# Kernel tuning notes

Measured on AMD Instinct MI355X. Metric: run time of the kernel, lower is better.

Reference implementation:

```python
import jax, jax.numpy as jnp
import numpy as np

DIM = 256
HEADS = 8
HEAD_DIM = DIM // HEADS
WS = 8
EPS = 1e-5


def layernorm(x, g, b):
    mu = jnp.mean(x, axis=-1, keepdims=True)
    var = jnp.var(x, axis=-1, keepdims=True)
    return (x - mu) * jax.lax.rsqrt(var + EPS) * g + b


def partition_windows(x, ws):
    B, H, W, C = x.shape
    x = x.reshape(B, H // ws, ws, W // ws, ws, C)
    x = jnp.transpose(x, (0, 1, 3, 2, 4, 5))
    return x.reshape(B * (H // ws) * (W // ws), ws * ws, C)


def unpartition_windows(x, ws, B, H, W):
    C = x.shape[-1]
    x = x.reshape(B, H // ws, W // ws, ws, ws, C)
    x = jnp.transpose(x, (0, 1, 3, 2, 4, 5))
    return x.reshape(B, H, W, C)


def setup_inputs() -> dict:
    key = jax.random.key(0)
    ks = jax.random.split(key, 14)
    B, H, W, C = 16, 64, 64, DIM
    s_in = 1.0 / np.sqrt(C)
    s_hid = 1.0 / np.sqrt(4 * C)
    return {
        "x": jax.random.normal(ks[0], (B, H, W, C), jnp.float32),
        "ln1_g": jnp.ones((C,), jnp.float32),
        "ln1_b": jnp.zeros((C,), jnp.float32),
        "qkv_w": jax.random.uniform(ks[1], (3 * C, C), jnp.float32, -s_in, s_in),
        "qkv_b": jax.random.uniform(ks[2], (3 * C,), jnp.float32, -s_in, s_in),
        "proj_w": jax.random.uniform(ks[3], (C, C), jnp.float32, -s_in, s_in),
        "proj_b": jax.random.uniform(ks[4], (C,), jnp.float32, -s_in, s_in),
        "ln2_g": jnp.ones((C,), jnp.float32),
        "ln2_b": jnp.zeros((C,), jnp.float32),
        "ffn_w1": jax.random.uniform(ks[5], (4 * C, C), jnp.float32, -s_in, s_in),
        "ffn_b1": jax.random.uniform(ks[6], (4 * C,), jnp.float32, -s_in, s_in),
        "ffn_w2": jax.random.uniform(ks[7], (C, 4 * C), jnp.float32, -s_hid, s_hid),
        "ffn_b2": jax.random.uniform(ks[8], (C,), jnp.float32, -s_hid, s_hid),
    }


def attention(blocks, qkv_w, qkv_b, proj_w, proj_b):
    # blocks: [Bn, N, C]
    Bn, N, C = blocks.shape
    qkv = blocks @ qkv_w.T + qkv_b  # [Bn, N, 3C]
    qkv = qkv.reshape(Bn, N, 3, HEADS, HEAD_DIM)
    q, k, v = qkv[:, :, 0], qkv[:, :, 1], qkv[:, :, 2]  # each [Bn, N, h, d]
    # Faithful to the source: q @ k^T over the last two dims -> head-x-head scores per token
    scores = jnp.einsum("bnhd,bngd->bnhg", q, k) / np.sqrt(HEAD_DIM)
    attn = jax.nn.softmax(scores, axis=-1)
    out = jnp.einsum("bnhg,bngd->bnhd", attn, v).reshape(Bn, N, C)
    return out @ proj_w.T + proj_b


def reference(x, ln1_g, ln1_b, qkv_w, qkv_b, proj_w, proj_b,
              ln2_g, ln2_b, ffn_w1, ffn_b1, ffn_w2, ffn_b2):
    B, H, W, C = x.shape
    x_ = layernorm(x, ln1_g, ln1_b)
    blocks = partition_windows(x_, WS)  # [B*nW, ws*ws, C]
    out = attention(blocks, qkv_w, qkv_b, proj_w, proj_b)
    x = x + unpartition_windows(out, WS, B, H, W)
    x_ = layernorm(x, ln2_g, ln2_b)
    x_ = jax.nn.relu(x_ @ ffn_w1.T + ffn_b1) @ ffn_w2.T + ffn_b2
    return x + x_
```

## Files before the change

kernel.cpp:

```cpp
#include <hip/hip_runtime.h>
#include <hip/hip_bf16.h>
#include <stdint.h>

typedef float f32x4 __attribute__((ext_vector_type(4)));
typedef __bf16 bf16x8 __attribute__((ext_vector_type(8)));
typedef unsigned short ushort8 __attribute__((ext_vector_type(8)));

__device__ __forceinline__ float bf2f(unsigned short u) {
    unsigned int x = ((unsigned int)u) << 16;
    return __builtin_bit_cast(float, x);
}
__device__ __forceinline__ unsigned short f2bf(float f) {
    unsigned int x = __builtin_bit_cast(unsigned int, f);
    unsigned int lsb = (x >> 16) & 1u;
    x += 0x7fffu + lsb;
    return (unsigned short)(x >> 16);
}

#define GLL16(gptr, lptr)                                                      \
    __builtin_amdgcn_global_load_lds(                                          \
        (const __attribute__((address_space(1))) void*)(gptr),                 \
        (__attribute__((address_space(3))) void*)(lptr), 16, 0, 0)

__global__ __launch_bounds__(256) void cvt4_kernel(
    const float* __restrict__ w0, const float* __restrict__ w1,
    const float* __restrict__ w2, const float* __restrict__ w3,
    unsigned short* __restrict__ dst)
{
    const int i = blockIdx.x * 256 + threadIdx.x;
    const float* s; int off;
    if      (i <  49152) { s = w0; off = 0; }
    else if (i <  65536) { s = w1; off = 49152; }
    else if (i < 131072) { s = w2; off = 65536; }
    else                 { s = w3; off = 131072; }
    f32x4 v = ((const f32x4*)s)[i - off];
    ushort4 o;
    o.x = f2bf(v.x); o.y = f2bf(v.y); o.z = f2bf(v.z); o.w = f2bf(v.w);
    ((ushort4*)dst)[i] = o;
}

__global__ __launch_bounds__(256) void ln_kernel(
    const float* __restrict__ x, const float* __restrict__ g,
    const float* __restrict__ b, unsigned short* __restrict__ y)
{
    const int lane = threadIdx.x & 63, wave = threadIdx.x >> 6;
    const size_t tok = (size_t)blockIdx.x * 4 + wave;
    f32x4 v = *(const f32x4*)(x + tok * 256 + lane * 4);
    float s = v.x + v.y + v.z + v.w;
    float q = v.x * v.x + v.y * v.y + v.z * v.z + v.w * v.w;
#pragma unroll
    for (int o = 32; o; o >>= 1) {
        s += __shfl_xor(s, o, 64);
        q += __shfl_xor(q, o, 64);
    }
    float mean = s * (1.f / 256.f);
    float var  = q * (1.f / 256.f) - mean * mean;
    float rstd = rsqrtf(var + 1e-5f);
    f32x4 gr = *(const f32x4*)(g + lane * 4);
    f32x4 br = *(const f32x4*)(b + lane * 4);
    ushort4 o4;
    o4.x = f2bf((v.x - mean) * rstd * gr.x + br.x);
    o4.y = f2bf((v.y - mean) * rstd * gr.y + br.y);
    o4.z = f2bf((v.z - mean) * rstd * gr.z + br.z);
    o4.w = f2bf((v.w - mean) * rstd * gr.w + br.w);
    *(ushort4*)(y + tok * 256 + lane * 4) = o4;
}

template <int RELU, int HASRES, int OUTF32>
__global__ __launch_bounds__(256) void gemm_bt(
    const unsigned short* __restrict__ A,
    const unsigned short* __restrict__ W,
    const float* __restrict__ bias,
    const float* res,
    void* Cv,
    int M, int N, int K, int nby)
{
    __shared__ __align__(16) unsigned short As[128 * 64];
    __shared__ __align__(16) unsigned short Bs[128 * 64];

    const int t    = threadIdx.x;
    const int id   = blockIdx.x;
    const int xcd  = id & 7;
    const int sl   = id >> 3;
    const int by   = sl % nby;
    const int bx   = (sl / nby) * 8 + xcd;
    const int m0   = bx * 128;
    const int n0   = by * 128;
    const int lane = t & 63;
    const int wave = t >> 6;
    const int wm = wave & 1, wn = wave >> 1;
    const int lr = lane & 15, kc = lane >> 4;

    f32x4 acc[4][4] = {};

    const int rA   = t >> 3;
    const int gcol = ((t & 7) ^ (rA & 7)) * 8;
    const unsigned short* gA = A + (size_t)(m0 + rA) * K + gcol;
    const unsigned short* gB = W + (size_t)(n0 + rA) * K + gcol;

    for (int k0 = 0; k0 < K; k0 += 64) {
#pragma unroll
        for (int w = 0; w < 4; ++w) {
            GLL16(gA + (size_t)(w * 32) * K + k0, &As[(w * 256 + t) * 8]);
            GLL16(gB + (size_t)(w * 32) * K + k0, &Bs[(w * 256 + t) * 8]);
        }
        __syncthreads();

#pragma unroll
        for (int hh = 0; hh < 2; ++hh) {
            bf16x8 af[4], bf[4];
#pragma unroll
            for (int i = 0; i < 4; ++i) {
                const int ra = wm * 64 + i * 16 + lr;
                const int rb = wn * 64 + i * 16 + lr;
                af[i] = *(const bf16x8*)&As[ra * 64 + ((hh * 4 + kc) ^ (ra & 7)) * 8];
                bf[i] = *(const bf16x8*)&Bs[rb * 64 + ((hh * 4 + kc) ^ (rb & 7)) * 8];
            }
#pragma unroll
            for (int i = 0; i < 4; ++i)
#pragma unroll
                for (int j = 0; j < 4; ++j)
                    acc[i][j] = __builtin_amdgcn_mfma_f32_16x16x32_bf16(
                        af[i], bf[j], acc[i][j], 0, 0, 0);
        }
        __syncthreads();
    }

    float* Cf = (float*)Cv;
    unsigned short* Cb = (unsigned short*)Cv;
    const int row0 = m0 + wm * 64;
    const int col0 = n0 + wn * 64;
    const int cl = lane & 15;
    const int rq = (lane >> 4) * 4;
#pragma unroll
    for (int i = 0; i < 4; ++i) {
#pragma unroll
        for (int j = 0; j < 4; ++j) {
            const int col = col0 + j * 16 + cl;
            const float bv = bias[col];
#pragma unroll
            for (int r = 0; r < 4; ++r) {
                const int row = row0 + i * 16 + rq + r;
                float v = acc[i][j][r] + bv;
                if (RELU) v = fmaxf(v, 0.f);
                const size_t o = (size_t)row * N + col;
                if (HASRES) v += res[o];
                if (OUTF32) Cf[o] = v;
                else        Cb[o] = f2bf(v);
            }
        }
    }
}

__global__ __launch_bounds__(256) void attn_headmix(
    const unsigned short* __restrict__ qkv,
    unsigned short* __restrict__ out,
    int T)
{
    const int lane = threadIdx.x & 63, wave = threadIdx.x >> 6;
    const int tok = blockIdx.x * 4 + wave;
    if (tok >= T) return;
    const unsigned short* base = qkv + (size_t)tok * 768;
    const int h = lane >> 3, g = lane & 7;

    float s = 0.f;
#pragma unroll
    for (int d8 = 0; d8 < 4; ++d8) {
        ushort4 qa = *(const ushort4*)(base + h * 32 + d8 * 8);
        ushort4 qb = *(const ushort4*)(base + h * 32 + d8 * 8 + 4);
        ushort4 ka = *(const ushort4*)(base + 256 + g * 32 + d8 * 8);
        ushort4 kb = *(const ushort4*)(base + 256 + g * 32 + d8 * 8 + 4);
        s += bf2f(qa.x) * bf2f(ka.x) + bf2f(qa.y) * bf2f(ka.y)
           + bf2f(qa.z) * bf2f(ka.z) + bf2f(qa.w) * bf2f(ka.w)
           + bf2f(qb.x) * bf2f(kb.x) + bf2f(qb.y) * bf2f(kb.y)
           + bf2f(qb.z) * bf2f(kb.z) + bf2f(qb.w) * bf2f(kb.w);
    }
    s *= 0.17677669529663687f;

    float mx = s;
#pragma unroll
    for (int o = 1; o < 8; o <<= 1) mx = fmaxf(mx, __shfl_xor(mx, o, 64));
    float e = __expf(s - mx);
    float sum = e;
#pragma unroll
    for (int o = 1; o < 8; o <<= 1) sum += __shfl_xor(sum, o, 64);
    const float a = e / sum;

    float o0 = 0.f, o1 = 0.f, o2 = 0.f, o3 = 0.f;
#pragma unroll
    for (int gg = 0; gg < 8; ++gg) {
        const float ag = __shfl(a, (lane & 56) | gg, 64);
        ushort4 vv = *(const ushort4*)(base + 512 + gg * 32 + g * 4);
        o0 += ag * bf2f(vv.x);
        o1 += ag * bf2f(vv.y);
        o2 += ag * bf2f(vv.z);
        o3 += ag * bf2f(vv.w);
    }
    ushort4 ov;
    ov.x = f2bf(o0); ov.y = f2bf(o1); ov.z = f2bf(o2); ov.w = f2bf(o3);
    *(ushort4*)(out + (size_t)tok * 256 + lane * 4) = ov;
}

__global__ __launch_bounds__(512, 2) void ffn_fused(
    float* xo,
    const float* __restrict__ ln2_g, const float* __restrict__ ln2_b,
    const unsigned short* __restrict__ w1,
    const float* __restrict__ b1p,
    const unsigned short* __restrict__ w2,
    const float* __restrict__ b2p)
{
    __shared__ __align__(16) unsigned short U[32768];
    __shared__ __align__(16) unsigned short W1a[16384];
    __shared__ __align__(16) unsigned short W2a[16384];
    __shared__ __align__(16) unsigned short Hs[128 * 72];

    unsigned short* const W1b = U;
    unsigned short* const W2b = U + 16384;

    const int t = threadIdx.x;
    const int lane = t & 63, wave = t >> 6;
    const int m0 = blockIdx.x * 128;
    const int lr = lane & 15, kc = lane >> 4;
    const int cl = lane & 15, rq = (lane >> 4) * 4;
    const int wm = wave & 1, wn = wave >> 1;

    const int r1b = t >> 5;
    const int sc1 = t & 31;
    const int gc1 = (sc1 & ~7) | ((sc1 & 7) ^ (r1b & 7));
    const int r2b = t >> 3;
    const int gc2 = (t & 7) ^ (r2b & 7);

    #define STAGE_W(hp, W1t, W2t)                                              \
        {                                                                      \
            _Pragma("unroll")                                                  \
            for (int j = 0; j < 4; ++j)                                        \
                GLL16(w1 + (size_t)((hp) * 64 + j * 16 + r1b) * 256 + gc1 * 8, \
                      &(W1t)[(j * 512 + t) * 8]);                              \
            _Pragma("unroll")                                                  \
            for (int j = 0; j < 4; ++j)                                        \
                GLL16(w2 + (size_t)(j * 64 + r2b) * 1024 + (hp) * 64 + gc2 * 8,\
                      &(W2t)[(j * 512 + t) * 8]);                              \
        }

    STAGE_W(0, W1a, W2a);

    {
        const int row0 = t >> 2;
        const int seg  = t & 3;
        const float* xrp = xo + (size_t)(m0 + row0) * 256 + seg * 64;
        f32x4 xv[16];
#pragma unroll
        for (int i = 0; i < 16; ++i) xv[i] = ((const f32x4*)xrp)[i];
        float s = 0.f, q = 0.f;
#pragma unroll
        for (int i = 0; i < 16; ++i) {
            s += xv[i].x + xv[i].y + xv[i].z + xv[i].w;
            q += xv[i].x * xv[i].x + xv[i].y * xv[i].y
               + xv[i].z * xv[i].z + xv[i].w * xv[i].w;
        }
        s += __shfl_xor(s, 1, 64); q += __shfl_xor(q, 1, 64);
        s += __shfl_xor(s, 2, 64); q += __shfl_xor(q, 2, 64);
        const float mean = s * (1.f / 256.f);
        const float rstd = rsqrtf(q * (1.f / 256.f) - mean * mean + 1e-5f);
#pragma unroll
        for (int c8 = 0; c8 < 8; ++c8) {
            const f32x4 g0 = ((const f32x4*)(ln2_g + seg * 64 + c8 * 8))[0];
            const f32x4 g1 = ((const f32x4*)(ln2_g + seg * 64 + c8 * 8))[1];
            const f32x4 bb0 = ((const f32x4*)(ln2_b + seg * 64 + c8 * 8))[0];
            const f32x4 bb1 = ((const f32x4*)(ln2_b + seg * 64 + c8 * 8))[1];
            const f32x4 a0 = xv[c8 * 2], a1 = xv[c8 * 2 + 1];
            ushort8 o;
            o[0] = f2bf((a0.x - mean) * rstd * g0.x + bb0.x);
            o[1] = f2bf((a0.y - mean) * rstd * g0.y + bb0.y);
            o[2] = f2bf((a0.z - mean) * rstd * g0.z + bb0.z);
            o[3] = f2bf((a0.w - mean) * rstd * g0.w + bb0.w);
            o[4] = f2bf((a1.x - mean) * rstd * g1.x + bb1.x);
            o[5] = f2bf((a1.y - mean) * rstd * g1.y + bb1.y);
            o[6] = f2bf((a1.z - mean) * rstd * g1.z + bb1.z);
            o[7] = f2bf((a1.w - mean) * rstd * g1.w + bb1.w);
            const int gc = seg * 8 + c8;
            const int sc = (gc & ~7) | ((gc & 7) ^ (row0 & 7));
            *(ushort8*)&U[row0 * 256 + sc * 8] = o;
        }
    }
    __syncthreads();

    bf16x8 afr[4][8];
#pragma unroll
    for (int i = 0; i < 4; ++i) {
        const int ra = wm * 64 + i * 16 + lr;
#pragma unroll
        for (int ks = 0; ks < 8; ++ks) {
            const int c = ks * 4 + kc;
            afr[i][ks] = *(const bf16x8*)
                &U[ra * 256 + ((c & ~7) | ((c & 7) ^ (ra & 7))) * 8];
        }
    }
    __syncthreads();
    STAGE_W(1, W1b, W2b);

    f32x4 acc[4][4] = {};

    for (int hc = 0; hc < 16; ++hc) {
        unsigned short* const W1c = (hc & 1) ? W1b : W1a;
        unsigned short* const W2c = (hc & 1) ? W2b : W2a;

        f32x4 acch[4] = {};
#pragma unroll
        for (int ks = 0; ks < 8; ++ks) {
            const int c = ks * 4 + kc;
            const int rb = wn * 16 + lr;
            const bf16x8 bfr = *(const bf16x8*)
                &W1c[rb * 256 + ((c & ~7) | ((c & 7) ^ (rb & 7))) * 8];
#pragma unroll
            for (int i = 0; i < 4; ++i)
                acch[i] = __builtin_amdgcn_mfma_f32_16x16x32_bf16(
                    afr[i][ks], bfr, acch[i], 0, 0, 0);
        }
        {
            const int hcol = wn * 16 + cl;
            const float bv1 = b1p[hc * 64 + hcol];
#pragma unroll
            for (int i = 0; i < 4; ++i)
#pragma unroll
                for (int r = 0; r < 4; ++r) {
                    const int hr = wm * 64 + i * 16 + rq + r;
                    Hs[hr * 72 + hcol] = f2bf(fmaxf(acch[i][r] + bv1, 0.f));
                }
        }
        __syncthreads();

#pragma unroll
        for (int ks = 0; ks < 2; ++ks) {
            const int c = ks * 4 + kc;
            bf16x8 bw[4];
#pragma unroll
            for (int j = 0; j < 4; ++j) {
                const int rb = wn * 64 + j * 16 + lr;
                bw[j] = *(const bf16x8*)&W2c[rb * 64 + ((c ^ (rb & 7)) * 8)];
            }
#pragma unroll
            for (int i = 0; i < 4; ++i) {
                const int ra = wm * 64 + i * 16 + lr;
                const bf16x8 ah = *(const bf16x8*)&Hs[ra * 72 + c * 8];
#pragma unroll
                for (int j = 0; j < 4; ++j)
                    acc[i][j] = __builtin_amdgcn_mfma_f32_16x16x32_bf16(
                        ah, bw[j], acc[i][j], 0, 0, 0);
            }
        }
        __syncthreads();
        if (hc < 14) STAGE_W(hc + 2, W1c, W2c);
    }

#pragma unroll
    for (int i = 0; i < 4; ++i)
#pragma unroll
        for (int j = 0; j < 4; ++j) {
            const int col = wn * 64 + j * 16 + cl;
            const float bv = b2p[col];
#pragma unroll
            for (int r = 0; r < 4; ++r) {
                const int row = m0 + wm * 64 + i * 16 + rq + r;
                const size_t o = (size_t)row * 256 + col;
                xo[o] = acc[i][j][r] + bv + xo[o];
            }
        }
    #undef STAGE_W
}

extern "C" void kernel_launch(void* const* d_in, const int* in_sizes, int n_in,
                              void* d_out, int out_size, void* d_ws, size_t ws_size,
                              hipStream_t stream)
{
    const float* x      = (const float*)d_in[0];
    const float* ln1_g  = (const float*)d_in[1];
    const float* ln1_b  = (const float*)d_in[2];
    const float* qkv_w  = (const float*)d_in[3];
    const float* qkv_b  = (const float*)d_in[4];
    const float* proj_w = (const float*)d_in[5];
    const float* proj_b = (const float*)d_in[6];
    const float* ln2_g  = (const float*)d_in[7];
    const float* ln2_b  = (const float*)d_in[8];
    const float* ffn_w1 = (const float*)d_in[9];
    const float* ffn_b1 = (const float*)d_in[10];
    const float* ffn_w2 = (const float*)d_in[11];
    const float* ffn_b2 = (const float*)d_in[12];
    float* xo = (float*)d_out;

    const int M = 65536;
    const size_t MEG = 1024 * 1024;
    unsigned short* ws = (unsigned short*)d_ws;
    unsigned short* qkv_wb  = ws;
    unsigned short* proj_wb = ws + 196608;
    unsigned short* ffn_w1b = ws + 262144;
    unsigned short* ffn_w2b = ws + 524288;
    unsigned short* xn   = ws + 1 * MEG;
    unsigned short* att  = ws + 17 * MEG;
    unsigned short* qkvb = ws + 33 * MEG;

    cvt4_kernel<<<768, 256, 0, stream>>>(qkv_w, proj_w, ffn_w1, ffn_w2, ws);

    ln_kernel<<<M / 4, 256, 0, stream>>>(x, ln1_g, ln1_b, xn);
    gemm_bt<0, 0, 0><<<3072, 256, 0, stream>>>(
        xn, qkv_wb, qkv_b, nullptr, qkvb, M, 768, 256, 6);
    attn_headmix<<<M / 4, 256, 0, stream>>>(qkvb, att, M);
    gemm_bt<0, 1, 1><<<1024, 256, 0, stream>>>(
        att, proj_wb, proj_b, x, xo, M, 256, 256, 2);
    ffn_fused<<<M / 128, 512, 0, stream>>>(
        xo, ln2_g, ln2_b, ffn_w1b, ffn_b1, ffn_w2b, ffn_b2);
}
```

Baseline: 399.7 us.

## Software-pipeline FFN hidden phase with double-buffered H tile and one barrier per step

Restructures the FFN loop so the first GEMM for the next hidden chunk runs alongside the second GEMM for the current chunk. The H tile is double-buffered, which cuts the loop to one barrier per iteration. The MFMA operands are swapped so each lane writes four contiguous bf16 values into an XOR-swizzled H layout instead of scattered scalar stores. It also adds s_setprio around the MFMA blocks and splits W1/W2 staging so they can be issued at different times. In exchange it uses more LDS and more registers, which may hurt occupancy, and the buffer reuse across stages is harder to verify.

New measurement: 413.7 us. 3.5% more time.

```diff
diff --git a/kernel.cpp b/kernel.cpp
--- a/kernel.cpp
+++ b/kernel.cpp
@@ -212,7 +212,7 @@
     __shared__ __align__(16) unsigned short U[32768];
     __shared__ __align__(16) unsigned short W1a[16384];
     __shared__ __align__(16) unsigned short W2a[16384];
-    __shared__ __align__(16) unsigned short Hs[128 * 72];
+    __shared__ __align__(16) unsigned short Hs[2][8192];
 
     unsigned short* const W1b = U;
     unsigned short* const W2b = U + 16384;
@@ -230,19 +230,23 @@
     const int r2b = t >> 3;
     const int gc2 = (t & 7) ^ (r2b & 7);
 
-    #define STAGE_W(hp, W1t, W2t)                                              \
-        {                                                                      \
+    #define STAGE_W1(hp, W1t)                                                  \
+        do {                                                                   \
             _Pragma("unroll")                                                  \
             for (int j = 0; j < 4; ++j)                                        \
                 GLL16(w1 + (size_t)((hp) * 64 + j * 16 + r1b) * 256 + gc1 * 8, \
                       &(W1t)[(j * 512 + t) * 8]);                              \
+        } while (0)
+    #define STAGE_W2(hp, W2t)                                                  \
+        do {                                                                   \
             _Pragma("unroll")                                                  \
             for (int j = 0; j < 4; ++j)                                        \
                 GLL16(w2 + (size_t)(j * 64 + r2b) * 1024 + (hp) * 64 + gc2 * 8,\
                       &(W2t)[(j * 512 + t) * 8]);                              \
-        }
-
-    STAGE_W(0, W1a, W2a);
+        } while (0)
+
+    STAGE_W1(0, W1a);
+    STAGE_W2(0, W2a);
 
     {
         const int row0 = t >> 2;
@@ -297,62 +301,80 @@
         }
     }
     __syncthreads();
-    STAGE_W(1, W1b, W2b);
+    STAGE_W1(1, W1b);
 
     f32x4 acc[4][4] = {};
 
+    #define HPHASE(hcv, W1c, Hbuf)                                             \
+        do {                                                                   \
+            f32x4 acch[4] = {};                                                \
+            __builtin_amdgcn_s_setprio(1);                                     \
+            _Pragma("unroll")                                                  \
+            for (int ks = 0; ks < 8; ++ks) {                                   \
+                const int c = ks * 4 + kc;                                     \
+                const int rb = wn * 16 + lr;                                   \
+                const bf16x8 bfr = *(const bf16x8*)                            \
+                    &(W1c)[rb * 256 + ((c & ~7) | ((c & 7) ^ (rb & 7))) * 8];  \
+                _Pragma("unroll")                                              \
+                for (int i = 0; i < 4; ++i)                                    \
+                    acch[i] = __builtin_amdgcn_mfma_f32_16x16x32_bf16(         \
+                        bfr, afr[i][ks], acch[i], 0, 0, 0);                    \
+            }                                                                  \
+            __builtin_amdgcn_s_setprio(0);                                     \
+            const f32x4 bv = *(const f32x4*)(b1p + (hcv) * 64 + wn * 16 + rq); \
+            const int sbase = wn * 2 + (rq >> 3);                              \
+            _Pragma("unroll")                                                  \
+            for (int i = 0; i < 4; ++i) {                                      \
+                const int tok = wm * 64 + i * 16 + cl;                         \
+                ushort4 o;                                                     \
+                o.x = f2bf(fmaxf(acch[i][0] + bv.x, 0.f));                     \
+                o.y = f2bf(fmaxf(acch[i][1] + bv.y, 0.f));                     \
+                o.z = f2bf(fmaxf(acch[i][2] + bv.z, 0.f));                     \
+                o.w = f2bf(fmaxf(acch[i][3] + bv.w, 0.f));                     \
+                *(ushort4*)&(Hbuf)[tok * 64 + ((sbase ^ (tok & 7)) * 8)        \
+                                   + (rq & 4)] = o;                            \
+            }                                                                  \
+        } while (0)
+
+    #define OPHASE(W2c, Hbuf)                                                  \
+        do {                                                                   \
+            _Pragma("unroll")                                                  \
+            for (int ks = 0; ks < 2; ++ks) {                                   \
+                const int c = ks * 4 + kc;                                     \
+                bf16x8 bw[4];                                                  \
+                _Pragma("unroll")                                              \
+                for (int j = 0; j < 4; ++j) {                                  \
+                    const int rb = wn * 64 + j * 16 + lr;                      \
+                    bw[j] = *(const bf16x8*)                                   \
+                        &(W2c)[rb * 64 + ((c ^ (rb & 7)) * 8)];                \
+                }                                                              \
+                __builtin_amdgcn_s_setprio(1);                                 \
+                _Pragma("unroll")                                              \
+                for (int i = 0; i < 4; ++i) {                                  \
+                    const int ra = wm * 64 + i * 16 + lr;                      \
+                    const bf16x8 ah = *(const bf16x8*)                         \
+                        &(Hbuf)[ra * 64 + ((c ^ (ra & 7)) * 8)];               \
+                    _Pragma("unroll")                                          \
+                    for (int j = 0; j < 4; ++j)                                \
+                        acc[i][j] = __builtin_amdgcn_mfma_f32_16x16x32_bf16(   \
+                            ah, bw[j], acc[i][j], 0, 0, 0);                    \
+                }                                                              \
+                __builtin_amdgcn_s_setprio(0);                                 \
+            }                                                                  \
+        } while (0)
+
+    HPHASE(0, W1a, Hs[0]);
+    __syncthreads();
+
     for (int hc = 0; hc < 16; ++hc) {
-        unsigned short* const W1c = (hc & 1) ? W1b : W1a;
-        unsigned short* const W2c = (hc & 1) ? W2b : W2a;
-
-        f32x4 acch[4] = {};
-#pragma unroll
-        for (int ks = 0; ks < 8; ++ks) {
-            const int c = ks * 4 + kc;
-            const int rb = wn * 16 + lr;
-            const bf16x8 bfr = *(const bf16x8*)
-                &W1c[rb * 256 + ((c & ~7) | ((c & 7) ^ (rb & 7))) * 8];
-#pragma unroll
-            for (int i = 0; i < 4; ++i)
-                acch[i] = __builtin_amdgcn_mfma_f32_16x16x32_bf16(
-                    afr[i][ks], bfr, acch[i], 0, 0, 0);
-        }
-        {
-            const int hcol = wn * 16 + cl;
-            const float bv1 = b1p[hc * 64 + hcol];
-#pragma unroll
-            for (int i = 0; i < 4; ++i)
-#pragma unroll
-                for (int r = 0; r < 4; ++r) {
-                    const int hr = wm * 64 + i * 16 + rq + r;
-                    Hs[hr * 72 + hcol] = f2bf(fmaxf(acch[i][r] + bv1, 0.f));
-                }
-        }
+        if (hc < 14) STAGE_W1(hc + 2, (hc & 1) ? W1b : W1a);
+        if (hc < 15) STAGE_W2(hc + 1, (hc & 1) ? W2a : W2b);
+        if (hc < 15) HPHASE(hc + 1, (hc & 1) ? W1a : W1b, Hs[(hc + 1) & 1]);
+        OPHASE((hc & 1) ? W2b : W2a, Hs[hc & 1]);
         __syncthreads();
-
-#pragma unroll
-        for (int ks = 0; ks < 2; ++ks) {
-            const int c = ks * 4 + kc;
-            bf16x8 bw[4];
-#pragma unroll
-            for (int j = 0; j < 4; ++j) {
-                const int rb = wn * 64 + j * 16 + lr;
-                bw[j] = *(const bf16x8*)&W2c[rb * 64 + ((c ^ (rb & 7)) * 8)];
-            }
-#pragma unroll
-            for (int i = 0; i < 4; ++i) {
-                const int ra = wm * 64 + i * 16 + lr;
-                const bf16x8 ah = *(const bf16x8*)&Hs[ra * 72 + c * 8];
-#pragma unroll
-                for (int j = 0; j < 4; ++j)
-                    acc[i][j] = __builtin_amdgcn_mfma_f32_16x16x32_bf16(
-                        ah, bw[j], acc[i][j], 0, 0, 0);
-            }
-        }
-        __syncthreads();
-        if (hc < 14) STAGE_W(hc + 2, W1c, W2c);
-    }
-
+    }
+
+    const int rqe = (lane >> 4) * 4;
 #pragma unroll
     for (int i = 0; i < 4; ++i)
 #pragma unroll
@@ -361,12 +383,15 @@
             const float bv = b2p[col];
 #pragma unroll
             for (int r = 0; r < 4; ++r) {
-                const int row = m0 + wm * 64 + i * 16 + rq + r;
+                const int row = m0 + wm * 64 + i * 16 + rqe + r;
                 const size_t o = (size_t)row * 256 + col;
                 xo[o] = acc[i][j][r] + bv + xo[o];
             }
         }
-    #undef STAGE_W
+    #undef STAGE_W1
+    #undef STAGE_W2
+    #undef HPHASE
+    #undef OPHASE
 }
 
 extern "C" void kernel_launch(void* const* d_in, const int* in_sizes, int n_in,
```

## Fuse head-mix attention into projection GEMM and retile FFN to 64-row blocks

Applied to the files above, without the earlier changes.

Replaces the separate attention kernel and projection GEMM with a single kernel that computes the head-mixing softmax per token straight into shared memory and then runs the projection MFMA against double-buffered weight tiles. This removes the bf16 attention intermediate's round trip through global memory and one launch. The fused FFN kernel is also retiled to 64 rows per block with 32-wide hidden chunks, a smaller LDS footprint, occupancy hint 4 and setprio around the MFMA loops, aiming for more resident blocks. The cost is less weight reuse per block and more barriers per hidden chunk.

New measurement: 360.3 us. 9.8% less time.

```diff
diff --git a/kernel.cpp b/kernel.cpp
--- a/kernel.cpp
+++ b/kernel.cpp
@@ -152,56 +152,138 @@
     }
 }
 
-__global__ __launch_bounds__(256) void attn_headmix(
+__global__ __launch_bounds__(512, 2) void proj_attn(
     const unsigned short* __restrict__ qkv,
-    unsigned short* __restrict__ out,
-    int T)
-{
-    const int lane = threadIdx.x & 63, wave = threadIdx.x >> 6;
-    const int tok = blockIdx.x * 4 + wave;
-    if (tok >= T) return;
-    const unsigned short* base = qkv + (size_t)tok * 768;
+    const unsigned short* __restrict__ wp,
+    const float* __restrict__ bias,
+    const float* __restrict__ res,
+    float* __restrict__ out)
+{
+    __shared__ __align__(16) unsigned short U[128 * 256];
+    __shared__ __align__(16) unsigned short Wk[2][16384];
+
+    const int t = threadIdx.x;
+    const int lane = t & 63, wave = t >> 6;
+    const int m0 = blockIdx.x * 128;
+    const int lr = lane & 15, kc = lane >> 4;
+    const int cl = lane & 15, rq = (lane >> 4) * 4;
+    const int wm = wave & 1, wn = wave >> 1;
+
+    const int r2b = t >> 3;
+    const int gc2 = (t & 7) ^ (r2b & 7);
+
+    #define STAGE_WP(kc4, Wt)                                                  \
+        do {                                                                   \
+            _Pragma("unroll")                                                  \
+            for (int j = 0; j < 4; ++j)                                        \
+                GLL16(wp + (size_t)(j * 64 + r2b) * 256 + (kc4) * 64 + gc2 * 8,\
+                      &(Wt)[(j * 512 + t) * 8]);                               \
+        } while (0)
+
+    STAGE_WP(0, Wk[0]);
+    STAGE_WP(1, Wk[1]);
+
     const int h = lane >> 3, g = lane & 7;
-
-    float s = 0.f;
-#pragma unroll
-    for (int d8 = 0; d8 < 4; ++d8) {
-        ushort4 qa = *(const ushort4*)(base + h * 32 + d8 * 8);
-        ushort4 qb = *(const ushort4*)(base + h * 32 + d8 * 8 + 4);
-        ushort4 ka = *(const ushort4*)(base + 256 + g * 32 + d8 * 8);
-        ushort4 kb = *(const ushort4*)(base + 256 + g * 32 + d8 * 8 + 4);
-        s += bf2f(qa.x) * bf2f(ka.x) + bf2f(qa.y) * bf2f(ka.y)
-           + bf2f(qa.z) * bf2f(ka.z) + bf2f(qa.w) * bf2f(ka.w)
-           + bf2f(qb.x) * bf2f(kb.x) + bf2f(qb.y) * bf2f(kb.y)
-           + bf2f(qb.z) * bf2f(kb.z) + bf2f(qb.w) * bf2f(kb.w);
-    }
-    s *= 0.17677669529663687f;
-
-    float mx = s;
-#pragma unroll
-    for (int o = 1; o < 8; o <<= 1) mx = fmaxf(mx, __shfl_xor(mx, o, 64));
-    float e = __expf(s - mx);
-    float sum = e;
-#pragma unroll
-    for (int o = 1; o < 8; o <<= 1) sum += __shfl_xor(sum, o, 64);
-    const float a = e / sum;
-
-    float o0 = 0.f, o1 = 0.f, o2 = 0.f, o3 = 0.f;
-#pragma unroll
-    for (int gg = 0; gg < 8; ++gg) {
-        const float ag = __shfl(a, (lane & 56) | gg, 64);
-        ushort4 vv = *(const ushort4*)(base + 512 + gg * 32 + g * 4);
-        o0 += ag * bf2f(vv.x);
-        o1 += ag * bf2f(vv.y);
-        o2 += ag * bf2f(vv.z);
-        o3 += ag * bf2f(vv.w);
-    }
-    ushort4 ov;
-    ov.x = f2bf(o0); ov.y = f2bf(o1); ov.z = f2bf(o2); ov.w = f2bf(o3);
-    *(ushort4*)(out + (size_t)tok * 256 + lane * 4) = ov;
-}
-
-__global__ __launch_bounds__(512, 2) void ffn_fused(
+    for (int p = 0; p < 16; ++p) {
+        const int row = p * 8 + wave;
+        const unsigned short* base = qkv + (size_t)(m0 + row) * 768;
+
+        float s = 0.f;
+#pragma unroll
+        for (int d8 = 0; d8 < 4; ++d8) {
+            ushort4 qa = *(const ushort4*)(base + h * 32 + d8 * 8);
+            ushort4 qb = *(const ushort4*)(base + h * 32 + d8 * 8 + 4);
+            ushort4 ka = *(const ushort4*)(base + 256 + g * 32 + d8 * 8);
+            ushort4 kb = *(const ushort4*)(base + 256 + g * 32 + d8 * 8 + 4);
+            s += bf2f(qa.x) * bf2f(ka.x) + bf2f(qa.y) * bf2f(ka.y)
+               + bf2f(qa.z) * bf2f(ka.z) + bf2f(qa.w) * bf2f(ka.w)
+               + bf2f(qb.x) * bf2f(kb.x) + bf2f(qb.y) * bf2f(kb.y)
+               + bf2f(qb.z) * bf2f(kb.z) + bf2f(qb.w) * bf2f(kb.w);
+        }
+        s *= 0.17677669529663687f;
+
+        float mx = s;
+#pragma unroll
+        for (int o = 1; o < 8; o <<= 1) mx = fmaxf(mx, __shfl_xor(mx, o, 64));
+        float e = __expf(s - mx);
+        float sum = e;
+#pragma unroll
+        for (int o = 1; o < 8; o <<= 1) sum += __shfl_xor(sum, o, 64);
+        const float a = e / sum;
+
+        float o0 = 0.f, o1 = 0.f, o2 = 0.f, o3 = 0.f;
+#pragma unroll
+        for (int gg = 0; gg < 8; ++gg) {
+            const float ag = __shfl(a, (lane & 56) | gg, 64);
+            ushort4 vv = *(const ushort4*)(base + 512 + gg * 32 + g * 4);
+            o0 += ag * bf2f(vv.x);
+            o1 += ag * bf2f(vv.y);
+            o2 += ag * bf2f(vv.z);
+            o3 += ag * bf2f(vv.w);
+        }
+        const int gcu = lane >> 1;
+        const int sc = (gcu & ~7) | ((gcu & 7) ^ (row & 7));
+        ushort4 ov;
+        ov.x = f2bf(o0); ov.y = f2bf(o1); ov.z = f2bf(o2); ov.w = f2bf(o3);
+        *(ushort4*)&U[row * 256 + sc * 8 + (lane & 1) * 4] = ov;
+    }
+    __syncthreads();
+
+    bf16x8 afr[4][8];
+#pragma unroll
+    for (int i = 0; i < 4; ++i) {
+        const int ra = wm * 64 + i * 16 + lr;
+#pragma unroll
+        for (int ks = 0; ks < 8; ++ks) {
+            const int c = ks * 4 + kc;
+            afr[i][ks] = *(const bf16x8*)
+                &U[ra * 256 + ((c & ~7) | ((c & 7) ^ (ra & 7))) * 8];
+        }
+    }
+
+    f32x4 acc[4][4] = {};
+    for (int c4 = 0; c4 < 4; ++c4) {
+        if (c4 >= 2) __syncthreads();
+        const unsigned short* Wc = Wk[c4 & 1];
+#pragma unroll
+        for (int kk = 0; kk < 2; ++kk) {
+            const int c = kk * 4 + kc;
+            bf16x8 bw[4];
+#pragma unroll
+            for (int j = 0; j < 4; ++j) {
+                const int rb = wn * 64 + j * 16 + lr;
+                bw[j] = *(const bf16x8*)&Wc[rb * 64 + ((c ^ (rb & 7)) * 8)];
+            }
+#pragma unroll
+            for (int i = 0; i < 4; ++i)
+#pragma unroll
+                for (int j = 0; j < 4; ++j)
+                    acc[i][j] = __builtin_amdgcn_mfma_f32_16x16x32_bf16(
+                        afr[i][c4 * 2 + kk], bw[j], acc[i][j], 0, 0, 0);
+        }
+        if (c4 < 2) {
+            __syncthreads();
+            STAGE_WP(c4 + 2, Wk[c4 & 1]);
+        }
+    }
+
+#pragma unroll
+    for (int i = 0; i < 4; ++i)
+#pragma unroll
+        for (int j = 0; j < 4; ++j) {
+            const int col = wn * 64 + j * 16 + cl;
+            const float bv = bias[col];
+#pragma unroll
+            for (int r = 0; r < 4; ++r) {
+                const int row = m0 + wm * 64 + i * 16 + rq + r;
+                const size_t o = (size_t)row * 256 + col;
+                out[o] = acc[i][j][r] + bv + res[o];
+            }
+        }
+    #undef STAGE_WP
+}
+
+__global__ __launch_bounds__(512, 4) void ffn_fused(
     float* xo,
     const float* __restrict__ ln2_g, const float* __restrict__ ln2_b,
     const unsigned short* __restrict__ w1,
@@ -209,65 +291,63 @@
     const unsigned short* __restrict__ w2,
     const float* __restrict__ b2p)
 {
-    __shared__ __align__(16) unsigned short U[32768];
-    __shared__ __align__(16) unsigned short W1a[16384];
-    __shared__ __align__(16) unsigned short W2a[16384];
-    __shared__ __align__(16) unsigned short Hs[128 * 72];
-
-    unsigned short* const W1b = U;
-    unsigned short* const W2b = U + 16384;
+    __shared__ __align__(16) unsigned short U[16384];
+    __shared__ __align__(16) unsigned short Hs[2048];
+
+    unsigned short* const W1c = U;
+    unsigned short* const W2c = U + 8192;
 
     const int t = threadIdx.x;
     const int lane = t & 63, wave = t >> 6;
-    const int m0 = blockIdx.x * 128;
+    const int m0 = blockIdx.x * 64;
     const int lr = lane & 15, kc = lane >> 4;
     const int cl = lane & 15, rq = (lane >> 4) * 4;
-    const int wm = wave & 1, wn = wave >> 1;
-
-    const int r1b = t >> 5;
-    const int sc1 = t & 31;
-    const int gc1 = (sc1 & ~7) | ((sc1 & 7) ^ (r1b & 7));
-    const int r2b = t >> 3;
-    const int gc2 = (t & 7) ^ (r2b & 7);
-
-    #define STAGE_W(hp, W1t, W2t)                                              \
-        {                                                                      \
-            _Pragma("unroll")                                                  \
-            for (int j = 0; j < 4; ++j)                                        \
-                GLL16(w1 + (size_t)((hp) * 64 + j * 16 + r1b) * 256 + gc1 * 8, \
-                      &(W1t)[(j * 512 + t) * 8]);                              \
-            _Pragma("unroll")                                                  \
-            for (int j = 0; j < 4; ++j)                                        \
-                GLL16(w2 + (size_t)(j * 64 + r2b) * 1024 + (hp) * 64 + gc2 * 8,\
-                      &(W2t)[(j * 512 + t) * 8]);                              \
-        }
-
-    STAGE_W(0, W1a, W2a);
+    const int wm = wave & 3, wh = wave >> 2;
+
+    const int si1a = t, si1b = 512 + t;
+    const int r1a = si1a >> 5, s1a = si1a & 31;
+    const int r1b_ = si1b >> 5, s1b = si1b & 31;
+    const int c1a = (s1a & ~7) | ((s1a & 7) ^ (r1a & 7));
+    const int c1b = (s1b & ~7) | ((s1b & 7) ^ (r1b_ & 7));
+    const int r2a = si1a >> 2, s2a = (si1a & 3) ^ ((r2a >> 1) & 3);
+    const int r2b = si1b >> 2, s2b = (si1b & 3) ^ ((r2b >> 1) & 3);
+
+    #define STAGE_W1(hp)                                                       \
+        do {                                                                   \
+            GLL16(w1 + (size_t)((hp) * 32 + r1a) * 256 + c1a * 8, &W1c[si1a * 8]); \
+            GLL16(w1 + (size_t)((hp) * 32 + r1b_) * 256 + c1b * 8, &W1c[si1b * 8]); \
+        } while (0)
+    #define STAGE_W2(hp)                                                       \
+        do {                                                                   \
+            GLL16(w2 + (size_t)r2a * 1024 + (hp) * 32 + s2a * 8, &W2c[si1a * 8]); \
+            GLL16(w2 + (size_t)r2b * 1024 + (hp) * 32 + s2b * 8, &W2c[si1b * 8]); \
+        } while (0)
 
     {
-        const int row0 = t >> 2;
-        const int seg  = t & 3;
-        const float* xrp = xo + (size_t)(m0 + row0) * 256 + seg * 64;
-        f32x4 xv[16];
-#pragma unroll
-        for (int i = 0; i < 16; ++i) xv[i] = ((const f32x4*)xrp)[i];
+        const int row0 = t >> 3;
+        const int seg  = t & 7;
+        const float* xrp = xo + (size_t)(m0 + row0) * 256 + seg * 32;
+        f32x4 xv[8];
+#pragma unroll
+        for (int i = 0; i < 8; ++i) xv[i] = ((const f32x4*)xrp)[i];
         float s = 0.f, q = 0.f;
 #pragma unroll
-        for (int i = 0; i < 16; ++i) {
+        for (int i = 0; i < 8; ++i) {
             s += xv[i].x + xv[i].y + xv[i].z + xv[i].w;
             q += xv[i].x * xv[i].x + xv[i].y * xv[i].y
                + xv[i].z * xv[i].z + xv[i].w * xv[i].w;
         }
         s += __shfl_xor(s, 1, 64); q += __shfl_xor(q, 1, 64);
         s += __shfl_xor(s, 2, 64); q += __shfl_xor(q, 2, 64);
+        s += __shfl_xor(s, 4, 64); q += __shfl_xor(q, 4, 64);
         const float mean = s * (1.f / 256.f);
         const float rstd = rsqrtf(q * (1.f / 256.f) - mean * mean + 1e-5f);
 #pragma unroll
-        for (int c8 = 0; c8 < 8; ++c8) {
-            const f32x4 g0 = ((const f32x4*)(ln2_g + seg * 64 + c8 * 8))[0];
-            const f32x4 g1 = ((const f32x4*)(ln2_g + seg * 64 + c8 * 8))[1];
-            const f32x4 bb0 = ((const f32x4*)(ln2_b + seg * 64 + c8 * 8))[0];
-            const f32x4 bb1 = ((const f32x4*)(ln2_b + seg * 64 + c8 * 8))[1];
+        for (int c8 = 0; c8 < 4; ++c8) {
+            const f32x4 g0 = ((const f32x4*)(ln2_g + seg * 32 + c8 * 8))[0];
+            const f32x4 g1 = ((const f32x4*)(ln2_g + seg * 32 + c8 * 8))[1];
+            const f32x4 bb0 = ((const f32x4*)(ln2_b + seg * 32 + c8 * 8))[0];
+            const f32x4 bb1 = ((const f32x4*)(ln2_b + seg * 32 + c8 * 8))[1];
             const f32x4 a0 = xv[c8 * 2], a1 = xv[c8 * 2 + 1];
             ushort8 o;
             o[0] = f2bf((a0.x - mean) * rstd * g0.x + bb0.x);
@@ -278,95 +358,84 @@
             o[5] = f2bf((a1.y - mean) * rstd * g1.y + bb1.y);
             o[6] = f2bf((a1.z - mean) * rstd * g1.z + bb1.z);
             o[7] = f2bf((a1.w - mean) * rstd * g1.w + bb1.w);
-            const int gc = seg * 8 + c8;
+            const int gc = seg * 4 + c8;
             const int sc = (gc & ~7) | ((gc & 7) ^ (row0 & 7));
             *(ushort8*)&U[row0 * 256 + sc * 8] = o;
         }
     }
     __syncthreads();
 
-    bf16x8 afr[4][8];
-#pragma unroll
-    for (int i = 0; i < 4; ++i) {
-        const int ra = wm * 64 + i * 16 + lr;
+    bf16x8 afr[8];
+#pragma unroll
+    for (int ks = 0; ks < 8; ++ks) {
+        const int ra = wm * 16 + lr;
+        const int c = ks * 4 + kc;
+        afr[ks] = *(const bf16x8*)
+            &U[ra * 256 + ((c & ~7) | ((c & 7) ^ (ra & 7))) * 8];
+    }
+    __syncthreads();
+
+    STAGE_W1(0);
+    STAGE_W2(0);
+    __syncthreads();
+
+    f32x4 acc[8] = {};
+
+    for (int hc = 0; hc < 32; ++hc) {
+        f32x4 acch = {};
+        __builtin_amdgcn_s_setprio(1);
 #pragma unroll
         for (int ks = 0; ks < 8; ++ks) {
             const int c = ks * 4 + kc;
-            afr[i][ks] = *(const bf16x8*)
-                &U[ra * 256 + ((c & ~7) | ((c & 7) ^ (ra & 7))) * 8];
-        }
-    }
-    __syncthreads();
-    STAGE_W(1, W1b, W2b);
-
-    f32x4 acc[4][4] = {};
-
-    for (int hc = 0; hc < 16; ++hc) {
-        unsigned short* const W1c = (hc & 1) ? W1b : W1a;
-        unsigned short* const W2c = (hc & 1) ? W2b : W2a;
-
-        f32x4 acch[4] = {};
-#pragma unroll
-        for (int ks = 0; ks < 8; ++ks) {
-            const int c = ks * 4 + kc;
-            const int rb = wn * 16 + lr;
+            const int rb = wh * 16 + lr;
             const bf16x8 bfr = *(const bf16x8*)
                 &W1c[rb * 256 + ((c & ~7) | ((c & 7) ^ (rb & 7))) * 8];
-#pragma unroll
-            for (int i = 0; i < 4; ++i)
-                acch[i] = __builtin_amdgcn_mfma_f32_16x16x32_bf16(
-                    afr[i][ks], bfr, acch[i], 0, 0, 0);
-        }
+            acch = __builtin_amdgcn_mfma_f32_16x16x32_bf16(bfr, afr[ks], acch, 0, 0, 0);
+        }
+        __builtin_amdgcn_s_setprio(0);
         {
-            const int hcol = wn * 16 + cl;
-            const float bv1 = b1p[hc * 64 + hcol];
-#pragma unroll
-            for (int i = 0; i < 4; ++i)
-#pragma unroll
-                for (int r = 0; r < 4; ++r) {
-                    const int hr = wm * 64 + i * 16 + rq + r;
-                    Hs[hr * 72 + hcol] = f2bf(fmaxf(acch[i][r] + bv1, 0.f));
-                }
+            const f32x4 bv = *(const f32x4*)(b1p + hc * 32 + wh * 16 + rq);
+            const int tok = wm * 16 + cl;
+            const int s0 = wh * 2 + (rq >> 3);
+            ushort4 o;
+            o.x = f2bf(fmaxf(acch[0] + bv.x, 0.f));
+            o.y = f2bf(fmaxf(acch[1] + bv.y, 0.f));
+            o.z = f2bf(fmaxf(acch[2] + bv.z, 0.f));
+            o.w = f2bf(fmaxf(acch[3] + bv.w, 0.f));
+            *(ushort4*)&Hs[tok * 32 + ((s0 ^ ((tok >> 1) & 3)) * 8) + (rq & 4)] = o;
         }
         __syncthreads();
-
-#pragma unroll
-        for (int ks = 0; ks < 2; ++ks) {
-            const int c = ks * 4 + kc;
-            bf16x8 bw[4];
-#pragma unroll
-            for (int j = 0; j < 4; ++j) {
-                const int rb = wn * 64 + j * 16 + lr;
-                bw[j] = *(const bf16x8*)&W2c[rb * 64 + ((c ^ (rb & 7)) * 8)];
-            }
-#pragma unroll
-            for (int i = 0; i < 4; ++i) {
-                const int ra = wm * 64 + i * 16 + lr;
-                const bf16x8 ah = *(const bf16x8*)&Hs[ra * 72 + c * 8];
-#pragma unroll
-                for (int j = 0; j < 4; ++j)
-                    acc[i][j] = __builtin_amdgcn_mfma_f32_16x16x32_bf16(
-                        ah, bw[j], acc[i][j], 0, 0, 0);
-            }
-        }
+        if (hc < 31) STAGE_W1(hc + 1);
+
+        const int ra = wm * 16 + lr;
+        const bf16x8 ah = *(const bf16x8*)
+            &Hs[ra * 32 + ((kc ^ ((ra >> 1) & 3)) * 8)];
+        __builtin_amdgcn_s_setprio(1);
+#pragma unroll
+        for (int j = 0; j < 8; ++j) {
+            const int rb = wh * 128 + j * 16 + lr;
+            const bf16x8 bw = *(const bf16x8*)
+                &W2c[rb * 32 + ((kc ^ ((rb >> 1) & 3)) * 8)];
+            acc[j] = __builtin_amdgcn_mfma_f32_16x16x32_bf16(ah, bw, acc[j], 0, 0, 0);
+        }
+        __builtin_amdgcn_s_setprio(0);
         __syncthreads();
-        if (hc < 14) STAGE_W(hc + 2, W1c, W2c);
-    }
-
-#pragma unroll
-    for (int i = 0; i < 4; ++i)
-#pragma unroll
-        for (int j = 0; j < 4; ++j) {
-            const int col = wn * 64 + j * 16 + cl;
-            const float bv = b2p[col];
-#pragma unroll
-            for (int r = 0; r < 4; ++r) {
-                const int row = m0 + wm * 64 + i * 16 + rq + r;
-                const size_t o = (size_t)row * 256 + col;
-                xo[o] = acc[i][j][r] + bv + xo[o];
-            }
-        }
-    #undef STAGE_W
+        if (hc < 31) STAGE_W2(hc + 1);
+    }
+
+#pragma unroll
+    for (int j = 0; j < 8; ++j) {
+        const int col = wh * 128 + j * 16 + cl;
+        const float bv = b2p[col];
+#pragma unroll
+        for (int r = 0; r < 4; ++r) {
+            const int row = m0 + wm * 16 + rq + r;
+            const size_t o = (size_t)row * 256 + col;
+            xo[o] = acc[j][r] + bv + xo[o];
+        }
+    }
+    #undef STAGE_W1
+    #undef STAGE_W2
 }
 
 extern "C" void kernel_launch(void* const* d_in, const int* in_sizes, int n_in,
@@ -396,7 +465,6 @@
     unsigned short* ffn_w1b = ws + 262144;
     unsigned short* ffn_w2b = ws + 524288;
     unsigned short* xn   = ws + 1 * MEG;
-    unsigned short* att  = ws + 17 * MEG;
     unsigned short* qkvb = ws + 33 * MEG;
 
     cvt4_kernel<<<768, 256, 0, stream>>>(qkv_w, proj_w, ffn_w1, ffn_w2, ws);
@@ -404,9 +472,8 @@
     ln_kernel<<<M / 4, 256, 0, stream>>>(x, ln1_g, ln1_b, xn);
     gemm_bt<0, 0, 0><<<3072, 256, 0, stream>>>(
         xn, qkv_wb, qkv_b, nullptr, qkvb, M, 768, 256, 6);
-    attn_headmix<<<M / 4, 256, 0, stream>>>(qkvb, att, M);
-    gemm_bt<0, 1, 1><<<1024, 256, 0, stream>>>(
-        att, proj_wb, proj_b, x, xo, M, 256, 256, 2);
-    ffn_fused<<<M / 128, 512, 0, stream>>>(
+    proj_attn<<<M / 128, 512, 0, stream>>>(
+        qkvb, proj_wb, proj_b, x, xo);
+    ffn_fused<<<M / 64, 512, 0, stream>>>(
         xo, ln2_g, ln2_b, ffn_w1b, ffn_b1, ffn_w2b, ffn_b2);
 }
```
